# Performance work log

Hardware: AMD Instinct MI355X
Metric: run time of the kernel (lower is better)

Reference implementation:

```python
import jax, jax.numpy as jnp
import numpy as np

B, T, C, H = 4, 4096, 2048, 128


def setup_inputs() -> dict:
    key = jax.random.key(0)
    ks = jax.random.split(key, 7)
    s = 0.02
    return {
        "x": jax.random.normal(ks[0], (B, T, C), dtype=jnp.float32),
        "Wk": jax.random.normal(ks[1], (C, H), dtype=jnp.float32) * s,
        "bk": jax.random.normal(ks[2], (H,), dtype=jnp.float32) * s,
        "Wq": jax.random.normal(ks[3], (C, H), dtype=jnp.float32) * s,
        "bq": jax.random.normal(ks[4], (H,), dtype=jnp.float32) * s,
        "Wv": jax.random.normal(ks[5], (C, H), dtype=jnp.float32) * s,
        "bv": jax.random.normal(ks[6], (H,), dtype=jnp.float32) * s,
    }


def reference(x, Wk, bk, Wq, bq, Wv, bv):
    # x: [B, T, C]
    Bq, Tq, Cq = x.shape
    k = x @ Wk + bk  # [B, T, H]
    q = x @ Wq + bq
    v = x @ Wv + bv
    # NOTE: original scales by C**-0.5 (input emb dim), faithfully reproduced.
    scale = jnp.asarray(Cq, x.dtype) ** -0.5
    wei = jnp.einsum("bth,bsh->bts", q, k) * scale  # [B, T, T]
    causal = jnp.tril(jnp.ones((Tq, Tq), dtype=bool))
    wei = jnp.where(causal, wei, -jnp.inf)
    wei = jax.nn.softmax(wei, axis=-1)
    # dropout omitted (inference/eval mode)
    return jnp.einsum("bts,bsh->bth", wei, v)  # [B, T, H]
```

## Files before the change

### kernel.cpp

```cpp
#include <hip/hip_runtime.h>
#include <hip/hip_bf16.h>
#include <stdint.h>

#define T_SEQ 4096
#define C_DIM 2048
#define H_DIM 128
#define NBATCH 4

typedef unsigned short u16;
typedef __attribute__((ext_vector_type(8))) __bf16 bf16x8;
typedef __attribute__((ext_vector_type(4))) float f32x4;
typedef __attribute__((ext_vector_type(8))) unsigned short u16x8;

__device__ __forceinline__ u16 f2bf(float f) {
  union { float f; uint32_t i; } v; v.f = f;
  uint32_t r = v.i + 0x7FFFu + ((v.i >> 16) & 1u);
  return (u16)(r >> 16);
}

__device__ __forceinline__ void gload16(const void* g, void* l) {
  __builtin_amdgcn_global_load_lds(
      (__attribute__((address_space(1))) void*)(g),
      (__attribute__((address_space(3))) void*)(l), 16, 0, 0);
}

__device__ __forceinline__ f32x4 mfma_bf16(bf16x8 a, bf16x8 b, f32x4 c) {
  return __builtin_amdgcn_mfma_f32_16x16x32_bf16(a, b, c, 0, 0, 0);
}

template<int CTRL>
__device__ __forceinline__ float dpp_mov(float x) {
  return __int_as_float(__builtin_amdgcn_mov_dpp(__float_as_int(x), CTRL, 0xF, 0xF, true));
}
__device__ __forceinline__ float red16_max(float v) {
  v = fmaxf(v, dpp_mov<0x121>(v));
  v = fmaxf(v, dpp_mov<0x122>(v));
  v = fmaxf(v, dpp_mov<0x124>(v));
  v = fmaxf(v, dpp_mov<0x128>(v));
  return v;
}
__device__ __forceinline__ float red16_sum(float v) {
  v += dpp_mov<0x121>(v);
  v += dpp_mov<0x122>(v);
  v += dpp_mov<0x124>(v);
  v += dpp_mov<0x128>(v);
  return v;
}

__global__ __launch_bounds__(256) void transpose_w(
    const float* __restrict__ Wq, const float* __restrict__ Wk,
    const float* __restrict__ Wv, u16* __restrict__ Wt)
{
  __shared__ u16 Wl[64 * 72];
  const int bk = blockIdx.x;
  const int bn = blockIdx.y;
  const int p  = blockIdx.z;
  const float* W = (p == 0) ? Wq : (p == 1) ? Wk : Wv;
  const int t = threadIdx.x;

  for (int ps = 0; ps < 16; ++ps) {
    int e  = ps * 256 + t;
    int kk = e >> 6, nn = e & 63;
    Wl[kk * 72 + nn] = f2bf(W[(size_t)(bk * 64 + kk) * H_DIM + bn * 64 + nn]);
  }
  __syncthreads();
  for (int ps = 0; ps < 16; ++ps) {
    int o  = ps * 256 + t;
    int nl = o >> 6, kl = o & 63;
    int n  = bn * 64 + nl;
    int g  = kl >> 3, j = kl & 7;
    int ks = ((g ^ (n & 7)) << 3) | j;
    Wt[(size_t)p * (H_DIM * C_DIM) + (size_t)n * C_DIM + bk * 64 + kl] = Wl[ks * 72 + nl];
  }
}

__global__ __launch_bounds__(512, 2) void qkv_fused(
    const float* __restrict__ x, const u16* __restrict__ Wt,
    const float* __restrict__ bq, const float* __restrict__ bk, const float* __restrict__ bv,
    u16* __restrict__ qo, u16* __restrict__ ko, u16* __restrict__ vTo)
{
  __shared__ alignas(16) u16 SMEM[28672];
  u16* As = SMEM;
  u16* Bs = SMEM + 4096;

  const int tid  = threadIdx.x;
  const int w    = tid >> 6, lane = tid & 63;
  const int t16  = lane & 15, quad = lane >> 4;
  const int mh   = w >> 2;
  const int nq   = w & 3;
  const int rt   = blockIdx.x;

  f32x4 acc[2][6];
  for (int i = 0; i < 2; ++i)
    for (int j = 0; j < 6; ++j) acc[i][j] = f32x4{0.f, 0.f, 0.f, 0.f};

  const size_t rowBase = (size_t)rt * 64;
  const int arow = tid >> 3;
  const int ag   = tid & 7;
  const float* xrow = &x[(rowBase + arow) * C_DIM + ag * 8];

  float4 a0 = ((const float4*)xrow)[0];
  float4 a1 = ((const float4*)xrow)[1];

  for (int k0 = 0; k0 < C_DIM; k0 += 64) {
    __syncthreads();
    for (int p = 0; p < 3; ++p) {
      const u16* Wp = Wt + (size_t)p * (H_DIM * C_DIM);
      for (int j = 0; j < 2; ++j) {
        int e8 = (((j << 3) + w) * 64 + lane) * 8;
        int rr = e8 >> 6, kk = e8 & 63;
        gload16(Wp + (size_t)rr * C_DIM + k0 + kk, &Bs[p * 8192 + e8]);
      }
    }
    {
      u16x8 pk;
      pk[0] = f2bf(a0.x); pk[1] = f2bf(a0.y); pk[2] = f2bf(a0.z); pk[3] = f2bf(a0.w);
      pk[4] = f2bf(a1.x); pk[5] = f2bf(a1.y); pk[6] = f2bf(a1.z); pk[7] = f2bf(a1.w);
      *(u16x8*)&As[arow * 64 + ((ag ^ (arow & 7)) << 3)] = pk;
    }
    if (k0 + 64 < C_DIM) {
      const float4* xp = (const float4*)(xrow + k0 + 64);
      a0 = xp[0]; a1 = xp[1];
    }
    __syncthreads();

    for (int ks = 0; ks < 2; ++ks) {
      bf16x8 af[2], bfr[6];
      for (int ra = 0; ra < 2; ++ra)
        af[ra] = *(const bf16x8*)&As[(mh * 32 + ra * 16 + t16) * 64 +
                                     (((ks * 4 + quad) ^ (t16 & 7)) << 3)];
      for (int c = 0; c < 6; ++c) {
        int col = nq * 96 + c * 16 + t16;
        int p = col >> 7, pc = col & 127;
        bfr[c] = *(const bf16x8*)&Bs[p * 8192 + pc * 64 +
                                     (((ks * 4 + quad) ^ (t16 & 7)) << 3)];
      }
      for (int ra = 0; ra < 2; ++ra)
        for (int c = 0; c < 6; ++c)
          acc[ra][c] = mfma_bf16(af[ra], bfr[c], acc[ra][c]);
    }
  }

  __syncthreads();
  u16* Oq = SMEM;
  u16* Ok = SMEM + 8192;
  u16* Ov = SMEM + 16384;

  for (int c = 0; c < 6; ++c) {
    int col = nq * 96 + c * 16 + t16;
    int p = col >> 7, pc = col & 127;
    float bias = (p == 0) ? bq[pc] : (p == 1) ? bk[pc] : bv[pc];
    for (int ra = 0; ra < 2; ++ra) {
      for (int r = 0; r < 4; ++r) {
        int row16 = mh * 32 + ra * 16 + quad * 4 + r;
        float v = acc[ra][c][r] + bias;
        if (p == 2) {
          int gt = row16 >> 3;
          Ov[pc * 64 + ((gt ^ (pc & 7)) << 3) + (row16 & 7)] = f2bf(v);
        } else {
          u16* O = (p == 0) ? Oq : Ok;
          int g = pc >> 3;
          O[row16 * 128 + (((g ^ (row16 & 15)) << 3) | (pc & 7))] = f2bf(v);
        }
      }
    }
  }
  __syncthreads();

  const int bb = rt >> 6;
  const int tb = (rt & 63) * 64;
  for (int ps = 0; ps < 2; ++ps) {
    int c = ps * 512 + tid;
    {
      int row16 = c >> 4, g = c & 15;
      u16x8 v = *(const u16x8*)&Oq[row16 * 128 + ((g ^ (row16 & 15)) << 3)];
      *(u16x8*)&qo[(rowBase + row16) * H_DIM + g * 8] = v;
    }
    *(u16x8*)&ko[rowBase * H_DIM + c * 8] = *(const u16x8*)&Ok[c * 8];
    {
      int d = c >> 3, gc = c & 7;
      *(u16x8*)&vTo[((size_t)bb * H_DIM + d) * T_SEQ + tb + gc * 8] =
          *(const u16x8*)&Ov[c * 8];
    }
  }
}

__global__ __launch_bounds__(256, 2) void flash_attn(
    const u16* __restrict__ q, const u16* __restrict__ k,
    const u16* __restrict__ vT, float* __restrict__ out,
    float* __restrict__ Opart, float* __restrict__ MLpart, int split)
{
  __shared__ alignas(16) u16 Kt[2][64 * 128];
  __shared__ alignas(16) u16 Vt[2][128 * 64];
  __shared__ alignas(16) u16 Ps[4 * 16 * 72];

  const int tid  = threadIdx.x;
  const int w    = tid >> 6, lane = tid & 63;
  const int t16  = lane & 15, quad = lane >> 4;
  const int b    = blockIdx.x;

  int qt, kt0, ktn, slot;
  if (split) {
    int bid = blockIdx.y;
    if (bid < 32)      { qt = 32 + bid; kt0 = 0;  ktn = 32;      slot = (b * 32 + bid) * 2; }
    else if (bid < 64) { qt = 95 - bid; kt0 = 32; ktn = qt - 31; slot = (b * 32 + (qt - 32)) * 2 + 1; }
    else               { qt = 95 - bid; kt0 = 0;  ktn = qt + 1;  slot = -1; }
  } else {
    qt = 63 - blockIdx.y; kt0 = 0; ktn = qt + 1; slot = -1;
  }

  const float SCALE = 0.022097086912079612f;
  const float L2E   = 1.4426950408889634f;

  bf16x8 qf[4];
  {
    const u16* qrow = q + ((size_t)(b * T_SEQ + qt * 64 + w * 16 + t16)) * H_DIM;
    for (int c = 0; c < 4; ++c)
      qf[c] = *(const bf16x8*)(qrow + c * 32 + quad * 8);
  }

  f32x4 Oc[8];
  for (int i = 0; i < 8; ++i) Oc[i] = f32x4{0.f, 0.f, 0.f, 0.f};
  float mrow[4] = {-1e30f, -1e30f, -1e30f, -1e30f};
  float lrow[4] = {0.f, 0.f, 0.f, 0.f};

  const u16* kbase = k  + ((size_t)b * T_SEQ) * H_DIM;
  const u16* vbase = vT + ((size_t)b * H_DIM) * T_SEQ;

  {
    const u16* kg = kbase + (size_t)(kt0 * 64) * H_DIM;
    for (int j = 0; j < 4; ++j) {
      int e8 = (((j << 2) + w) * 64 + lane) * 8;
      gload16(kg + e8, &Kt[0][e8]);
      int d = e8 >> 6, kk = e8 & 63;
      gload16(vbase + (size_t)d * T_SEQ + kt0 * 64 + kk, &Vt[0][e8]);
    }
  }

  int cur = 0;
  for (int it = 0; it < ktn; ++it) {
    const int kt = kt0 + it;
    __syncthreads();
    if (it + 1 < ktn) {
      const int nb = cur ^ 1, ktn1 = kt + 1;
      const u16* kg = kbase + (size_t)(ktn1 * 64) * H_DIM;
      for (int j = 0; j < 4; ++j) {
        int e8 = (((j << 2) + w) * 64 + lane) * 8;
        gload16(kg + e8, &Kt[nb][e8]);
        int d = e8 >> 6, kk = e8 & 63;
        gload16(vbase + (size_t)d * T_SEQ + ktn1 * 64 + kk, &Vt[nb][e8]);
      }
    }

    f32x4 S[4];
    for (int ct = 0; ct < 4; ++ct) S[ct] = f32x4{0.f, 0.f, 0.f, 0.f};
    for (int c = 0; c < 4; ++c) {
      for (int ct = 0; ct < 4; ++ct) {
        bf16x8 kf = *(const bf16x8*)&Kt[cur][(ct * 16 + t16) * H_DIM +
                                            (((c * 4 + quad) ^ t16) << 3)];
        S[ct] = mfma_bf16(qf[c], kf, S[ct]);
      }
    }

    const bool diag = (kt == qt);
    for (int ct = 0; ct < 4; ++ct)
      for (int r = 0; r < 4; ++r) {
        float s = S[ct][r] * SCALE;
        if (diag && (ct * 16 + t16 > w * 16 + quad * 4 + r)) s = -1e30f;
        S[ct][r] = s;
      }

    float alpha[4], mnew[4];
    for (int r = 0; r < 4; ++r) {
      float mx = red16_max(fmaxf(fmaxf(S[0][r], S[1][r]), fmaxf(S[2][r], S[3][r])));
      mnew[r]  = fmaxf(mrow[r], mx);
      alpha[r] = exp2f((mrow[r] - mnew[r]) * L2E);
      mrow[r]  = mnew[r];
    }
    for (int r = 0; r < 4; ++r) {
      float s = 0.f;
      for (int ct = 0; ct < 4; ++ct) {
        float pv = exp2f((S[ct][r] - mnew[r]) * L2E);
        S[ct][r] = pv;
        s += pv;
      }
      lrow[r] = lrow[r] * alpha[r] + red16_sum(s);
    }
    for (int dt = 0; dt < 8; ++dt)
      for (int r = 0; r < 4; ++r)
        Oc[dt][r] *= alpha[r];

    u16* pw = &Ps[w * 1152];
    for (int ct = 0; ct < 4; ++ct)
      for (int r = 0; r < 4; ++r)
        pw[(quad * 4 + r) * 72 + ct * 16 + t16] = f2bf(S[ct][r]);
    __asm__ volatile("s_waitcnt lgkmcnt(0)" ::: "memory");

    for (int ks = 0; ks < 2; ++ks) {
      bf16x8 pf = *(const bf16x8*)&pw[t16 * 72 + ks * 32 + quad * 8];
      for (int dt = 0; dt < 8; ++dt) {
        bf16x8 vf = *(const bf16x8*)&Vt[cur][(dt * 16 + t16) * 64 +
                                            (((ks * 4 + quad) ^ (t16 & 7)) << 3)];
        Oc[dt] = mfma_bf16(pf, vf, Oc[dt]);
      }
    }
    cur ^= 1;
  }

  if (slot < 0) {
    for (int r = 0; r < 4; ++r) {
      float inv = 1.0f / lrow[r];
      size_t row = (size_t)b * T_SEQ + qt * 64 + w * 16 + quad * 4 + r;
      for (int dt = 0; dt < 8; ++dt)
        out[row * H_DIM + dt * 16 + t16] = Oc[dt][r] * inv;
    }
  } else {
    if (t16 == 0) {
      for (int r = 0; r < 4; ++r) {
        int row = w * 16 + quad * 4 + r;
        MLpart[(size_t)slot * 128 + row * 2 + 0] = mrow[r];
        MLpart[(size_t)slot * 128 + row * 2 + 1] = lrow[r];
      }
    }
    float* op = Opart + (size_t)slot * 8192;
    for (int r = 0; r < 4; ++r) {
      int row = w * 16 + quad * 4 + r;
      for (int dt = 0; dt < 8; ++dt)
        op[row * 128 + dt * 16 + t16] = Oc[dt][r];
    }
  }
}

__global__ __launch_bounds__(256) void combine(
    const float* __restrict__ Opart, const float* __restrict__ MLpart,
    float* __restrict__ out)
{
  __shared__ float c1s[64], c2s[64];
  const float L2E = 1.4426950408889634f;
  const int s = blockIdx.x;
  const int b = s >> 5, qt = 32 + (s & 31);
  const int t = threadIdx.x;

  if (t < 64) {
    const float* ML1 = MLpart + (size_t)(s * 2) * 128;
    const float* ML2 = ML1 + 128;
    float m1 = ML1[t * 2], l1 = ML1[t * 2 + 1];
    float m2 = ML2[t * 2], l2 = ML2[t * 2 + 1];
    float m  = fmaxf(m1, m2);
    float e1 = exp2f((m1 - m) * L2E);
    float e2 = exp2f((m2 - m) * L2E);
    float inv = 1.0f / (l1 * e1 + l2 * e2);
    c1s[t] = e1 * inv; c2s[t] = e2 * inv;
  }
  __syncthreads();

  const float* O1 = Opart + (size_t)(s * 2) * 8192;
  const float* O2 = O1 + 8192;
  float* o = out + ((size_t)b * T_SEQ + qt * 64) * (size_t)H_DIM;
  for (int i = t; i < 8192; i += 256) {
    int row = i >> 7;
    o[i] = O1[i] * c1s[row] + O2[i] * c2s[row];
  }
}

extern "C" void kernel_launch(void* const* d_in, const int* in_sizes, int n_in,
                              void* d_out, int out_size, void* d_ws, size_t ws_size,
                              hipStream_t stream) {
  const float* x  = (const float*)d_in[0];
  const float* Wk = (const float*)d_in[1];
  const float* bk = (const float*)d_in[2];
  const float* Wq = (const float*)d_in[3];
  const float* bq = (const float*)d_in[4];
  const float* Wv = (const float*)d_in[5];
  const float* bv = (const float*)d_in[6];
  float* out = (float*)d_out;

  char* ws = (char*)d_ws;
  u16* qb  = (u16*)(ws);
  u16* kb  = (u16*)(ws + 4194304);
  u16* vT  = (u16*)(ws + 8388608);
  u16* Wt  = (u16*)(ws + 12582912);
  float* Opart  = (float*)(ws + 14155776);
  float* MLpart = (float*)(ws + 14155776 + 8388608);

  const size_t need = 14155776ull + 8388608ull + 131072ull;
  const int split = (ws_size >= need) ? 1 : 0;

  hipLaunchKernelGGL(transpose_w, dim3(32, 2, 3), dim3(256), 0, stream, Wq, Wk, Wv, Wt);
  hipLaunchKernelGGL(qkv_fused, dim3(256), dim3(512), 0, stream,
                     x, Wt, bq, bk, bv, qb, kb, vT);
  hipLaunchKernelGGL(flash_attn, dim3(4, split ? 96 : 64), dim3(256), 0, stream,
                     qb, kb, vT, out, Opart, MLpart, split);
  if (split)
    hipLaunchKernelGGL(combine, dim3(128), dim3(256), 0, stream, Opart, MLpart, out);
}
```

Measured before the change: 310.4 us.

## Double-buffer LDS tiles in QKV projection GEMM to overlap loads with MFMA

The QKV projection kernel now keeps two LDS buffers. It prefetches the next K-slab of weights (async global-to-LDS) and the converted x tile while computing MFMAs on the current slab, which cuts one barrier per iteration. LDS use doubles to about 112KB, so launch bounds drop from 2 to 1 block per CU. That reduces occupancy and latency hiding across blocks in exchange for overlap within each block.

New measurement: 295.6 us. 4.8% less time.

```diff
diff --git a/kernel.cpp b/kernel.cpp
--- a/kernel.cpp
+++ b/kernel.cpp
@@ -74,14 +74,12 @@
   }
 }
 
-__global__ __launch_bounds__(512, 2) void qkv_fused(
+__global__ __launch_bounds__(512, 1) void qkv_fused(
     const float* __restrict__ x, const u16* __restrict__ Wt,
     const float* __restrict__ bq, const float* __restrict__ bk, const float* __restrict__ bv,
     u16* __restrict__ qo, u16* __restrict__ ko, u16* __restrict__ vTo)
 {
-  __shared__ alignas(16) u16 SMEM[28672];
-  u16* As = SMEM;
-  u16* Bs = SMEM + 4096;
+  __shared__ alignas(16) u16 SMEM[2][28672];
 
   const int tid  = threadIdx.x;
   const int w    = tid >> 6, lane = tid & 63;
@@ -99,31 +97,56 @@
   const int ag   = tid & 7;
   const float* xrow = &x[(rowBase + arow) * C_DIM + ag * 8];
 
-  float4 a0 = ((const float4*)xrow)[0];
-  float4 a1 = ((const float4*)xrow)[1];
-
-  for (int k0 = 0; k0 < C_DIM; k0 += 64) {
-    __syncthreads();
+
+  float4 a0 = ((const float4*)(xrow))[0];
+  float4 a1 = ((const float4*)(xrow))[1];
+  {
+    u16* As = SMEM[0];
+    u16* Bs = SMEM[0] + 4096;
     for (int p = 0; p < 3; ++p) {
       const u16* Wp = Wt + (size_t)p * (H_DIM * C_DIM);
       for (int j = 0; j < 2; ++j) {
         int e8 = (((j << 3) + w) * 64 + lane) * 8;
         int rr = e8 >> 6, kk = e8 & 63;
-        gload16(Wp + (size_t)rr * C_DIM + k0 + kk, &Bs[p * 8192 + e8]);
-      }
-    }
-    {
+        gload16(Wp + (size_t)rr * C_DIM + kk, &Bs[p * 8192 + e8]);
+      }
+    }
+    u16x8 pk;
+    pk[0] = f2bf(a0.x); pk[1] = f2bf(a0.y); pk[2] = f2bf(a0.z); pk[3] = f2bf(a0.w);
+    pk[4] = f2bf(a1.x); pk[5] = f2bf(a1.y); pk[6] = f2bf(a1.z); pk[7] = f2bf(a1.w);
+    *(u16x8*)&As[arow * 64 + ((ag ^ (arow & 7)) << 3)] = pk;
+  }
+  a0 = ((const float4*)(xrow + 64))[0];
+  a1 = ((const float4*)(xrow + 64))[1];
+
+  for (int it = 0; it < 32; ++it) {
+    const int cur = it & 1, nxt = cur ^ 1;
+    __syncthreads();
+
+    if (it + 1 < 32) {
+      const int k1 = (it + 1) * 64;
+      u16* As = SMEM[nxt];
+      u16* Bs = SMEM[nxt] + 4096;
+      for (int p = 0; p < 3; ++p) {
+        const u16* Wp = Wt + (size_t)p * (H_DIM * C_DIM);
+        for (int j = 0; j < 2; ++j) {
+          int e8 = (((j << 3) + w) * 64 + lane) * 8;
+          int rr = e8 >> 6, kk = e8 & 63;
+          gload16(Wp + (size_t)rr * C_DIM + k1 + kk, &Bs[p * 8192 + e8]);
+        }
+      }
       u16x8 pk;
       pk[0] = f2bf(a0.x); pk[1] = f2bf(a0.y); pk[2] = f2bf(a0.z); pk[3] = f2bf(a0.w);
       pk[4] = f2bf(a1.x); pk[5] = f2bf(a1.y); pk[6] = f2bf(a1.z); pk[7] = f2bf(a1.w);
       *(u16x8*)&As[arow * 64 + ((ag ^ (arow & 7)) << 3)] = pk;
-    }
-    if (k0 + 64 < C_DIM) {
-      const float4* xp = (const float4*)(xrow + k0 + 64);
-      a0 = xp[0]; a1 = xp[1];
-    }
-    __syncthreads();
-
+      if (it + 2 < 32) {
+        const float4* xp = (const float4*)(xrow + (it + 2) * 64);
+        a0 = xp[0]; a1 = xp[1];
+      }
+    }
+
+    u16* As = SMEM[cur];
+    u16* Bs = SMEM[cur] + 4096;
     for (int ks = 0; ks < 2; ++ks) {
       bf16x8 af[2], bfr[6];
       for (int ra = 0; ra < 2; ++ra)
@@ -142,9 +165,9 @@
   }
 
   __syncthreads();
-  u16* Oq = SMEM;
-  u16* Ok = SMEM + 8192;
-  u16* Ov = SMEM + 16384;
+  u16* Oq = SMEM[0];
+  u16* Ok = SMEM[0] + 8192;
+  u16* Ov = SMEM[0] + 16384;
 
   for (int c = 0; c < 6; ++c) {
     int col = nq * 96 + c * 16 + t16;
```
